# Kernel optimization log

Hardware: AMD Instinct MI355X
Metric: run time of the kernel (lower is better)

## Reference

```python
import jax, jax.numpy as jnp
import numpy as np

NUM_C = 100
DIM_S = 128
SIZE_M = 64
EMB = 128
MAX_CODE_LEN = 128
NODE_COUNT = 10000
PATH_COUNT = 10000
B, L = 16, 128


def setup_inputs() -> dict:
    key = jax.random.key(0)
    ks = jax.random.split(key, 24)
    def nrm(k, shape, fan):
        return jax.random.normal(k, shape, jnp.float32) * np.float32(np.sqrt(2.0 / fan))
    code = jax.random.randint(ks[0], (B, L, NUM_C * 2 + MAX_CODE_LEN * 3), 0, 10000)
    q = jax.random.randint(ks[1], (B, L), 0, NUM_C)
    r = jax.random.randint(ks[2], (B, L), 0, 2 * NUM_C)
    return {
        "code": code, "q": q, "r": r,
        "embed_nodes": nrm(ks[3], (NODE_COUNT + 2, EMB), EMB),
        "embed_paths": nrm(ks[4], (PATH_COUNT + 2, EMB), EMB),
        "W_pt": nrm(ks[5], (3 * EMB, 3 * EMB), 3 * EMB), "b_pt": jnp.zeros((3 * EMB,), jnp.float32),
        "W_att": nrm(ks[6], (3 * EMB, 1), 3 * EMB), "b_att": jnp.zeros((1,), jnp.float32),
        "k_emb": nrm(ks[7], (NUM_C + 1, DIM_S), DIM_S),
        "Mk": nrm(ks[8], (SIZE_M, DIM_S), DIM_S),
        "Mv0": nrm(ks[9], (SIZE_M, DIM_S), DIM_S),
        "v_emb": nrm(ks[10], (NUM_C * 2 + 2, DIM_S), DIM_S),
        "W_e": nrm(ks[11], (4 * DIM_S, DIM_S), 4 * DIM_S), "b_e": jnp.zeros((DIM_S,), jnp.float32),
        "W_a": nrm(ks[12], (4 * DIM_S, DIM_S), 4 * DIM_S), "b_a": jnp.zeros((DIM_S,), jnp.float32),
        "W_f": nrm(ks[13], (2 * DIM_S, DIM_S), 2 * DIM_S), "b_f": jnp.zeros((DIM_S,), jnp.float32),
        "W_p": nrm(ks[14], (DIM_S, 10), DIM_S), "b_p": jnp.zeros((10,), jnp.float32),
    }


def reference(code, q, r, embed_nodes, embed_paths, W_pt, b_pt, W_att, b_att,
              k_emb, Mk, Mv0, v_emb, W_e, b_e, W_a, b_a, W_f, b_f, W_p, b_p):
    bsz = code.shape[0]
    k = k_emb[q]                                    # [B,L,D]
    vr = v_emb[r]                                   # [B,L,D]
    # code2vec path triples: [B,L,MAX_CODE_LEN,3] = (start, path, end)
    c2v = code[:, :, NUM_C * 2:].reshape(bsz, code.shape[1], MAX_CODE_LEN, 3)
    full = jnp.concatenate([embed_nodes[c2v[..., 0]],
                            embed_nodes[c2v[..., 2]],
                            embed_paths[c2v[..., 1]]], axis=3)   # [B,L,P,3E]
    tr = jnp.tanh(full @ W_pt + b_pt)
    cw = tr @ W_att + b_att                          # [B,L,P,1]
    attn = jax.nn.softmax(cw, axis=1)                # faithful: softmax over seq dim (dim=1)
    code_vec = jnp.sum(full * attn, axis=2)          # [B,L,3E]
    v = jnp.concatenate([vr, code_vec], axis=2)      # [B,L,4D]
    w = jax.nn.softmax(k @ Mk.T, axis=-1)            # [B,L,M]
    e = jax.nn.sigmoid(v @ W_e + b_e)                # [B,L,D]
    a = jnp.tanh(v @ W_a + b_a)                      # [B,L,D]
    Mvt0 = jnp.broadcast_to(Mv0, (bsz,) + Mv0.shape) # [B,M,D]

    def step(Mvt, inp):
        et, at, wt = inp                             # [B,D],[B,D],[B,M]
        read = jnp.einsum('bm,bmd->bd', wt, Mvt)     # read pre-update memory (Mv[:, :-1])
        Mvt = Mvt * (1.0 - wt[:, :, None] * et[:, None, :]) + wt[:, :, None] * at[:, None, :]
        return Mvt, read

    _, reads = jax.lax.scan(step, Mvt0,
                            (e.transpose(1, 0, 2), a.transpose(1, 0, 2), w.transpose(1, 0, 2)))
    read = reads.transpose(1, 0, 2)                  # [B,L,D]
    f = jnp.tanh(jnp.concatenate([read, k], axis=-1) @ W_f + b_f)
    # dropout is identity in eval mode
    return jax.nn.sigmoid(f @ W_p + b_p)             # [B,L,10]
```

## Files before the change

kernel.cpp:

```cpp
#include <hip/hip_runtime.h>


typedef unsigned char u8;
typedef unsigned short u16;
typedef unsigned int u32;
typedef __attribute__((ext_vector_type(8))) short short8;
typedef __attribute__((ext_vector_type(4))) float f32x4;
typedef __attribute__((ext_vector_type(2))) float f32x2;

#define DEV __device__ __forceinline__
#define LOG2E 1.4426950408889634f
#define KSCALE 2.8853900817779268f

DEV u16 f2b(float f) {
    union { float f; u32 i; } v; v.f = f;
    u32 x = v.i;
    u32 r = (x + 0x7FFFu + ((x >> 16) & 1u)) >> 16;
    return (u16)r;
}
DEV float nexp(float x) { return __builtin_amdgcn_exp2f(x * LOG2E); }
DEV float nrcp(float x) { return __builtin_amdgcn_rcpf(x); }
DEV float fast_tanh(float x) {
    return 1.f - 2.f * nrcp(1.f + __builtin_amdgcn_exp2f(x * (2.f * LOG2E)));
}
DEV float sigmoidf_(float x) { return nrcp(1.f + __builtin_amdgcn_exp2f(-x * LOG2E)); }
DEV f32x2 d8(u32 x, bool hi) {
    return hi ? __builtin_amdgcn_cvt_pk_f32_fp8((int)x, true)
              : __builtin_amdgcn_cvt_pk_f32_fp8((int)x, false);
}
DEV u8 e8(float x) {
    return (u8)(__builtin_amdgcn_cvt_pk_fp8_f32(x, x, 0, false) & 0xFF);
}

__global__ void k_conv(const float* __restrict__ EN, const float* __restrict__ EP,
                       const float* __restrict__ Wpt, const float* __restrict__ We,
                       const float* __restrict__ Wa, const float* __restrict__ Wf,
                       const float* __restrict__ Wp,
                       const float* __restrict__ Kemb, const float* __restrict__ Mk,
                       u16* __restrict__ ENb, u16* __restrict__ EPb,
                       u8* __restrict__ EN8, u8* __restrict__ EP8,
                       u16* __restrict__ Wt, u16* __restrict__ WeaT,
                       u16* __restrict__ WfT, u16* __restrict__ WpT,
                       float* __restrict__ wsmall) {
    if (blockIdx.x >= 2048) {
        int wv = threadIdx.x >> 6, lane = threadIdx.x & 63;
        int row = (blockIdx.x - 2048) * 4 + wv;
        if (row >= 101) return;
        float lg = 0.f;
        for (int k = 0; k < 128; k += 8) {
            float mk8[8];
#pragma unroll
            for (int u = 0; u < 8; u++) mk8[u] = Mk[lane * 128 + k + u];
#pragma unroll
            for (int u = 0; u < 8; u++) lg = fmaf(Kemb[row * 128 + k + u], mk8[u], lg);
        }
        float mx = lg;
#pragma unroll
        for (int off = 32; off; off >>= 1) mx = fmaxf(mx, __shfl_xor(mx, off, 64));
        float ex = nexp(lg - mx);
        float sum = ex;
#pragma unroll
        for (int off = 32; off; off >>= 1) sum += __shfl_xor(sum, off, 64);
        wsmall[row * 64 + lane] = ex * nrcp(sum);
        return;
    }
    const int NEH = 10002 * 64;
    const int T0 = 2 * NEH;
    const int T1 = T0 + 147456;
    const int T2 = T1 + 131072;
    const int T3 = T2 + 32768;
    const int T4 = T3 + 2048;
    for (int i = blockIdx.x * blockDim.x + threadIdx.x; i < T4; i += 2048 * blockDim.x) {
        if (i < NEH) {
            float a = EN[2 * i], b = EN[2 * i + 1];
            ((u32*)ENb)[i] = ((u32)f2b(b) << 16) | f2b(a);
            ((u16*)EN8)[i] = (u16)__builtin_amdgcn_cvt_pk_fp8_f32(a, b, 0, false);
        } else if (i < T0) {
            int j = i - NEH;
            float a = EP[2 * j], b = EP[2 * j + 1];
            ((u32*)EPb)[j] = ((u32)f2b(b) << 16) | f2b(a);
            ((u16*)EP8)[j] = (u16)__builtin_amdgcn_cvt_pk_fp8_f32(a, b, 0, false);
        } else if (i < T1) {
            int w = i - T0;  u32 n = (u32)w / 384u, k = (u32)w % 384u;
            Wt[w] = f2b(Wpt[k * 384 + n]);
        } else if (i < T2) {
            int w = i - T1;  int n = w >> 9, k = w & 511;
            WeaT[w] = f2b((n < 128) ? We[k * 128 + n] : Wa[k * 128 + (n - 128)]);
        } else if (i < T3) {
            int w = i - T2;  int n = w >> 8, k = w & 255;
            WfT[w] = f2b(Wf[k * 128 + n]);
        } else {
            int w = i - T3;  int n = w >> 7, k = w & 127;
            WpT[w] = (n < 10) ? f2b(Wp[k * 10 + n]) : (u16)0;
        }
    }
}

__global__ void k_preM(const u16* __restrict__ ENb, const u16* __restrict__ EPb,
                       const u16* __restrict__ Wt, const float* __restrict__ bpt,
                       u8* __restrict__ PS8, u8* __restrict__ PE8, u8* __restrict__ PP8) {
    int which = blockIdx.y;
    int r0 = blockIdx.x * 32;
    int wv = threadIdx.x >> 6, lane = threadIdx.x & 63;
    int m = lane & 15, quad = lane >> 4;
    const u16* A = (which == 2) ? EPb : ENb;
    int koff = which * 128;
    u8* dst = (which == 0) ? PS8 : (which == 1) ? PE8 : PP8;

    short8 a[2][4];
#pragma unroll
    for (int rt = 0; rt < 2; rt++) {
        const short8* ap = (const short8*)(A + (r0 + rt * 16 + m) * 128 + quad * 8);
#pragma unroll
        for (int kc = 0; kc < 4; kc++) a[rt][kc] = ap[kc * 4];
    }

    for (int nt = 0; nt < 6; nt++) {
        int n0 = wv * 96 + nt * 16;
        const short8* bp = (const short8*)(Wt + (n0 + m) * 384 + koff + quad * 8);
        short8 b0 = bp[0], b1 = bp[4], b2 = bp[8], b3 = bp[12];
        int col = n0 + m;
        float bias = (which == 2) ? bpt[col] : 0.f;
#pragma unroll
        for (int rt = 0; rt < 2; rt++) {
            f32x4 acc = {0.f, 0.f, 0.f, 0.f};
            acc = __builtin_amdgcn_mfma_f32_16x16x32_bf16(a[rt][0], b0, acc, 0, 0, 0);
            acc = __builtin_amdgcn_mfma_f32_16x16x32_bf16(a[rt][1], b1, acc, 0, 0, 0);
            acc = __builtin_amdgcn_mfma_f32_16x16x32_bf16(a[rt][2], b2, acc, 0, 0, 0);
            acc = __builtin_amdgcn_mfma_f32_16x16x32_bf16(a[rt][3], b3, acc, 0, 0, 0);
#pragma unroll
            for (int reg = 0; reg < 4; reg++) {
                int row = r0 + rt * 16 + quad * 4 + reg;
                if (row < 10002) dst[row * 384 + col] = e8((acc[reg] + bias) * KSCALE);
            }
        }
    }
}

__global__ void k_cwsm(const int* __restrict__ code,
                       const u8* __restrict__ PS8, const u8* __restrict__ PE8,
                       const u8* __restrict__ PP8, const float* __restrict__ Watt,
                       float* __restrict__ attn) {
    int bp = blockIdx.x;
    int b = bp >> 7, p = bp & 127;
    int tid = threadIdx.x;
    int g = tid >> 4, gl = tid & 15;
    __shared__ float lgs[128];
    __shared__ float redm[4], reds[4];

    float w24[24];
    const float4* wp = (const float4*)(Watt + gl * 24);
#pragma unroll
    for (int u = 0; u < 6; u++) {
        float4 f = wp[u];
        w24[4 * u + 0] = -2.f * f.x; w24[4 * u + 1] = -2.f * f.y;
        w24[4 * u + 2] = -2.f * f.z; w24[4 * u + 3] = -2.f * f.w;
    }

    int si[8], pi[8], ei[8];
#pragma unroll
    for (int it = 0; it < 8; it++) {
        const int* c = code + ((b * 128 + g + it * 16) * 584 + 200 + 3 * p);
        si[it] = c[0]; pi[it] = c[1]; ei[it] = c[2];
    }

    uint2 cs0, cs1, cs2, ce0, ce1, ce2, cq0, cq1, cq2;
    {
        const uint2* bs = (const uint2*)(PS8 + si[0] * 384 + gl * 24);
        const uint2* be = (const uint2*)(PE8 + ei[0] * 384 + gl * 24);
        const uint2* bq = (const uint2*)(PP8 + pi[0] * 384 + gl * 24);
        cs0 = bs[0]; cs1 = bs[1]; cs2 = bs[2];
        ce0 = be[0]; ce1 = be[1]; ce2 = be[2];
        cq0 = bq[0]; cq1 = bq[1]; cq2 = bq[2];
    }
#pragma unroll
    for (int it = 0; it < 8; it++) {
        uint2 ns0, ns1, ns2, ne0, ne1, ne2, nq0, nq1, nq2;
        if (it < 7) {
            const uint2* bs = (const uint2*)(PS8 + si[it + 1] * 384 + gl * 24);
            const uint2* be = (const uint2*)(PE8 + ei[it + 1] * 384 + gl * 24);
            const uint2* bq = (const uint2*)(PP8 + pi[it + 1] * 384 + gl * 24);
            ns0 = bs[0]; ns1 = bs[1]; ns2 = bs[2];
            ne0 = be[0]; ne1 = be[1]; ne2 = be[2];
            nq0 = bq[0]; nq1 = bq[1]; nq2 = bq[2];
        }
        u32 sv[6] = { cs0.x, cs0.y, cs1.x, cs1.y, cs2.x, cs2.y };
        u32 ev[6] = { ce0.x, ce0.y, ce1.x, ce1.y, ce2.x, ce2.y };
        u32 qv[6] = { cq0.x, cq0.y, cq1.x, cq1.y, cq2.x, cq2.y };
        float acc = 0.f;
#pragma unroll
        for (int u = 0; u < 6; u++) {
            f32x2 zl = d8(sv[u], false) + d8(ev[u], false) + d8(qv[u], false);
            f32x2 zh = d8(sv[u], true)  + d8(ev[u], true)  + d8(qv[u], true);
            acc = fmaf(nrcp(1.f + __builtin_amdgcn_exp2f(zl.x)), w24[4 * u + 0], acc);
            acc = fmaf(nrcp(1.f + __builtin_amdgcn_exp2f(zl.y)), w24[4 * u + 1], acc);
            acc = fmaf(nrcp(1.f + __builtin_amdgcn_exp2f(zh.x)), w24[4 * u + 2], acc);
            acc = fmaf(nrcp(1.f + __builtin_amdgcn_exp2f(zh.y)), w24[4 * u + 3], acc);
        }
        acc += __shfl_xor(acc, 1, 64);
        acc += __shfl_xor(acc, 2, 64);
        acc += __shfl_xor(acc, 4, 64);
        acc += __shfl_xor(acc, 8, 64);
        if (gl == 0) lgs[g + it * 16] = acc;
        if (it < 7) {
            cs0 = ns0; cs1 = ns1; cs2 = ns2;
            ce0 = ne0; ce1 = ne1; ce2 = ne2;
            cq0 = nq0; cq1 = nq1; cq2 = nq2;
        }
    }
    __syncthreads();

    int lane = tid & 63, wvi = tid >> 6;
    float x = (tid < 128) ? lgs[tid] : -1e30f;
    float mx = x;
#pragma unroll
    for (int off = 32; off; off >>= 1) mx = fmaxf(mx, __shfl_xor(mx, off, 64));
    if (lane == 0) redm[wvi] = mx;
    __syncthreads();
    mx = fmaxf(redm[0], redm[1]);
    float ex = nexp(x - mx);
    float sum = ex;
#pragma unroll
    for (int off = 32; off; off >>= 1) sum += __shfl_xor(sum, off, 64);
    if (lane == 0) reds[wvi] = sum;
    __syncthreads();
    float inv = nrcp(reds[0] + reds[1]);
    if (tid < 128) attn[(b * 128 + tid) * 128 + p] = ex * inv;
}

__global__ void k_cv(const int* __restrict__ code, const float* __restrict__ attn,
                     const u8* __restrict__ EN8, const u8* __restrict__ EP8,
                     const int* __restrict__ rr, const int* __restrict__ qq,
                     const float* __restrict__ Vemb, const float* __restrict__ Kemb,
                     u16* __restrict__ vA, u16* __restrict__ fA) {
    int row = blockIdx.x;
    int tid = threadIdx.x;
    int wv = tid >> 6, lane = tid & 63;
    __shared__ int si[128], ei[128], pi[128];
    __shared__ float at[128];
    __shared__ float part[4][3][128];
    if (tid < 128) {
        const int* c = code + (row * 584 + 200);
        si[tid] = c[3 * tid]; pi[tid] = c[3 * tid + 1]; ei[tid] = c[3 * tid + 2];
        at[tid] = attn[row * 128 + tid];
    }
    if (tid < 128) {
        vA[row * 512 + tid] = f2b(Vemb[rr[row] * 128 + tid]);
    } else {
        int t2 = tid - 128;
        fA[row * 256 + 128 + t2] = f2b(Kemb[qq[row] * 128 + t2]);
    }
    __syncthreads();
    float a0 = 0.f, a1 = 0.f, b0 = 0.f, b1 = 0.f, c0 = 0.f, c1 = 0.f;
    int o = 2 * lane;

    u32 cur[6];
    {
        int p = wv, p2 = wv + 4;
        cur[0] = *(const u16*)(EN8 + si[p] * 128 + o);
        cur[1] = *(const u16*)(EN8 + ei[p] * 128 + o);
        cur[2] = *(const u16*)(EP8 + pi[p] * 128 + o);
        cur[3] = *(const u16*)(EN8 + si[p2] * 128 + o);
        cur[4] = *(const u16*)(EN8 + ei[p2] * 128 + o);
        cur[5] = *(const u16*)(EP8 + pi[p2] * 128 + o);
    }
#pragma unroll
    for (int it = 0; it < 16; it++) {
        int p = wv + it * 8;
        u32 nxt[6];
        if (it < 15) {
            int pn = p + 8, pn2 = p + 12;
            nxt[0] = *(const u16*)(EN8 + si[pn] * 128 + o);
            nxt[1] = *(const u16*)(EN8 + ei[pn] * 128 + o);
            nxt[2] = *(const u16*)(EP8 + pi[pn] * 128 + o);
            nxt[3] = *(const u16*)(EN8 + si[pn2] * 128 + o);
            nxt[4] = *(const u16*)(EN8 + ei[pn2] * 128 + o);
            nxt[5] = *(const u16*)(EP8 + pi[pn2] * 128 + o);
        }
        float w = at[p], w2 = at[p + 4];
        f32x2 fs = d8(cur[0], false), fe = d8(cur[1], false), fp = d8(cur[2], false);
        f32x2 gs = d8(cur[3], false), ge = d8(cur[4], false), gp = d8(cur[5], false);
        a0 = fmaf(w, fs.x, a0); a1 = fmaf(w, fs.y, a1);
        b0 = fmaf(w, fe.x, b0); b1 = fmaf(w, fe.y, b1);
        c0 = fmaf(w, fp.x, c0); c1 = fmaf(w, fp.y, c1);
        a0 = fmaf(w2, gs.x, a0); a1 = fmaf(w2, gs.y, a1);
        b0 = fmaf(w2, ge.x, b0); b1 = fmaf(w2, ge.y, b1);
        c0 = fmaf(w2, gp.x, c0); c1 = fmaf(w2, gp.y, c1);
        if (it < 15) {
#pragma unroll
            for (int z = 0; z < 6; z++) cur[z] = nxt[z];
        }
    }
    part[wv][0][2 * lane] = a0; part[wv][0][2 * lane + 1] = a1;
    part[wv][1][2 * lane] = b0; part[wv][1][2 * lane + 1] = b1;
    part[wv][2][2 * lane] = c0; part[wv][2][2 * lane + 1] = c1;
    __syncthreads();
    u16* vrow = vA + row * 512 + 128;
    for (int idx = tid; idx < 384; idx += 256) {
        int tbl = idx >> 7, col = idx & 127;
        vrow[idx] = f2b(part[0][tbl][col] + part[1][tbl][col] + part[2][tbl][col] + part[3][tbl][col]);
    }
}

__global__ void k_eawM(const u16* __restrict__ vA, const u16* __restrict__ WeaT,
                       const float* __restrict__ be, const float* __restrict__ ba,
                       float* __restrict__ eb, float* __restrict__ ab) {
    int rt = blockIdx.x >> 2, cg = blockIdx.x & 3;
    int wv = threadIdx.x >> 6, lane = threadIdx.x & 63;
    int ct = cg * 4 + wv;
    int m = lane & 15, quad = lane >> 4;
    const short8* ap = (const short8*)(vA + (rt * 16 + m) * 512 + quad * 8);
    const short8* bp = (const short8*)(WeaT + (ct * 16 + m) * 512 + quad * 8);
    f32x4 acc = {0.f, 0.f, 0.f, 0.f};
#pragma unroll
    for (int kc = 0; kc < 16; kc++)
        acc = __builtin_amdgcn_mfma_f32_16x16x32_bf16(ap[kc * 4], bp[kc * 4], acc, 0, 0, 0);
    int col = ct * 16 + m;
    bool isA = col >= 128;
    int c2 = isA ? col - 128 : col;
    float bias = isA ? ba[c2] : be[c2];
#pragma unroll
    for (int reg = 0; reg < 4; reg++) {
        int row = rt * 16 + quad * 4 + reg;
        float val = acc[reg] + bias;
        if (isA) ab[row * 128 + c2] = fast_tanh(val);
        else     eb[row * 128 + c2] = sigmoidf_(val);
    }
}

__global__ void k_scan(const float* __restrict__ Mv0, const float* __restrict__ eb,
                       const float* __restrict__ ab, const float* __restrict__ wsmall,
                       const int* __restrict__ qq, u16* __restrict__ fA) {
    int b = blockIdx.x >> 4, dblk = blockIdx.x & 15;
    int lane = threadIdx.x;
    int s = lane >> 3, dlo = lane & 7;
    int d = dblk * 8 + dlo;

    __shared__ float wsm[101 * 64];
    __shared__ float el[128][8];
    __shared__ float al[128][8];
    __shared__ int ql[128];

    for (int i = lane; i < 101 * 64; i += 64) wsm[i] = wsmall[i];
    for (int i = lane; i < 1024; i += 64) {
        int t = i >> 3, dl = i & 7;
        el[t][dl] = eb[(b * 128 + t) * 128 + dblk * 8 + dl];
        al[t][dl] = ab[(b * 128 + t) * 128 + dblk * 8 + dl];
    }
    for (int i = lane; i < 128; i += 64) ql[i] = qq[b * 128 + i];
    __syncthreads();

    float mv[8];
#pragma unroll
    for (int q = 0; q < 8; q++) mv[q] = Mv0[(s * 8 + q) * 128 + d];

    u16* fout = fA + (b * 128) * 256 + d;

    int qt = ql[0];
    const float4* wr = (const float4*)(wsm + qt * 64 + s * 8);
    float4 w0 = wr[0], w1 = wr[1];
    float ecur = el[0][dlo], acur = al[0][dlo];

    for (int t = 0; t < 128; t++) {
        int tn = (t < 127) ? t + 1 : 127;
        int qn = ql[tn];
        const float4* wrn = (const float4*)(wsm + qn * 64 + s * 8);
        float4 nw0 = wrn[0], nw1 = wrn[1];
        float en = el[tn][dlo], an = al[tn][dlo];

        float w[8] = { w0.x, w0.y, w0.z, w0.w, w1.x, w1.y, w1.z, w1.w };
        float rd = 0.f;
#pragma unroll
        for (int q = 0; q < 8; q++) {
            rd = fmaf(w[q], mv[q], rd);
            mv[q] = fmaf(w[q], fmaf(-mv[q], ecur, acur), mv[q]);
        }
        rd += __shfl_xor(rd, 8, 64);
        rd += __shfl_xor(rd, 16, 64);
        rd += __shfl_xor(rd, 32, 64);
        if (s == 0) fout[t * 256] = f2b(rd);

        ecur = en; acur = an; w0 = nw0; w1 = nw1;
    }
}

__global__ void k_outfin(const u16* __restrict__ fA, const u16* __restrict__ WfT,
                         const float* __restrict__ bfp, const u16* __restrict__ WpT,
                         const float* __restrict__ bp, float* __restrict__ out) {
    int rt = blockIdx.x;
    int wv = threadIdx.x >> 6, lane = threadIdx.x & 63;
    int m = lane & 15, quad = lane >> 4;
    __shared__ u16 ftile[16][128];

    const short8* ap = (const short8*)(fA + (rt * 16 + m) * 256 + quad * 8);
    const short8* bpw = (const short8*)(WfT + (wv * 16 + m) * 256 + quad * 8);
    f32x4 acc = {0.f, 0.f, 0.f, 0.f};
#pragma unroll
    for (int kc = 0; kc < 8; kc++)
        acc = __builtin_amdgcn_mfma_f32_16x16x32_bf16(ap[kc * 4], bpw[kc * 4], acc, 0, 0, 0);
    int col = wv * 16 + m;
    float bias = bfp[col];
#pragma unroll
    for (int reg = 0; reg < 4; reg++)
        ftile[quad * 4 + reg][col] = f2b(fast_tanh(acc[reg] + bias));
    __syncthreads();

    if (wv == 0) {
        f32x4 facc = {0.f, 0.f, 0.f, 0.f};
#pragma unroll
        for (int kc = 0; kc < 4; kc++) {
            short8 af = *(const short8*)(&ftile[m][kc * 32 + quad * 8]);
            short8 bf = *(const short8*)(WpT + m * 128 + kc * 32 + quad * 8);
            facc = __builtin_amdgcn_mfma_f32_16x16x32_bf16(af, bf, facc, 0, 0, 0);
        }
        if (m < 10) {
            float bias2 = bp[m];
#pragma unroll
            for (int reg = 0; reg < 4; reg++) {
                int row = rt * 16 + quad * 4 + reg;
                out[row * 10 + m] = sigmoidf_(facc[reg] + bias2);
            }
        }
    }
}

extern "C" void kernel_launch(void* const* d_in, const int* in_sizes, int n_in,
                              void* d_out, int out_size, void* d_ws, size_t ws_size,
                              hipStream_t stream) {
    const int*   code = (const int*)d_in[0];
    const int*   q    = (const int*)d_in[1];
    const int*   r    = (const int*)d_in[2];
    const float* EN   = (const float*)d_in[3];
    const float* EP   = (const float*)d_in[4];
    const float* Wpt  = (const float*)d_in[5];
    const float* bpt  = (const float*)d_in[6];
    const float* Watt = (const float*)d_in[7];
    const float* Kemb = (const float*)d_in[9];
    const float* Mk   = (const float*)d_in[10];
    const float* Mv0  = (const float*)d_in[11];
    const float* Vemb = (const float*)d_in[12];
    const float* We   = (const float*)d_in[13];
    const float* be   = (const float*)d_in[14];
    const float* Wa   = (const float*)d_in[15];
    const float* ba   = (const float*)d_in[16];
    const float* Wf   = (const float*)d_in[17];
    const float* bf_  = (const float*)d_in[18];
    const float* Wp   = (const float*)d_in[19];
    const float* bp   = (const float*)d_in[20];

    char* ws = (char*)d_ws;
    size_t off = 0;
    auto alloc = [&](size_t bytes) { void* p = ws + off; off = (off + bytes + 255) & ~255UL; return p; };
    u8*    PS8    = (u8*)alloc(10002UL * 384);
    u8*    PE8    = (u8*)alloc(10002UL * 384);
    u8*    PP8    = (u8*)alloc(10002UL * 384);
    u16*   ENb    = (u16*)alloc(10016UL * 128 * 2);
    u16*   EPb    = (u16*)alloc(10016UL * 128 * 2);
    u8*    EN8    = (u8*)alloc(10002UL * 128);
    u8*    EP8    = (u8*)alloc(10002UL * 128);
    u16*   Wt     = (u16*)alloc(384UL * 384 * 2);
    u16*   WeaT   = (u16*)alloc(256UL * 512 * 2);
    u16*   WfT    = (u16*)alloc(128UL * 256 * 2);
    u16*   WpT    = (u16*)alloc(16UL * 128 * 2);
    float* attn   = (float*)alloc(16UL * 128 * 128 * 4);
    u16*   vA     = (u16*)alloc(2048UL * 512 * 2);
    u16*   fA     = (u16*)alloc(2048UL * 256 * 2);
    float* eb     = (float*)alloc(2048UL * 128 * 4);
    float* ab     = (float*)alloc(2048UL * 128 * 4);
    float* wsmall = (float*)alloc(101UL * 64 * 4);

    k_conv<<<2048 + 26, 256, 0, stream>>>(EN, EP, Wpt, We, Wa, Wf, Wp, Kemb, Mk,
                                          ENb, EPb, EN8, EP8, Wt, WeaT, WfT, WpT, wsmall);
    k_preM<<<dim3(313, 3), 256, 0, stream>>>(ENb, EPb, Wt, bpt, PS8, PE8, PP8);
    k_cwsm<<<2048, 256, 0, stream>>>(code, PS8, PE8, PP8, Watt, attn);
    k_cv<<<2048, 256, 0, stream>>>(code, attn, EN8, EP8, r, q, Vemb, Kemb, vA, fA);
    k_eawM<<<512, 256, 0, stream>>>(vA, WeaT, be, ba, eb, ab);
    k_scan<<<256, 64, 0, stream>>>(Mv0, eb, ab, wsmall, q, fA);
    k_outfin<<<128, 512, 0, stream>>>(fA, WfT, bf_, WpT, bp, (float*)d_out);
}
```

Before: 224.0 us.

## Widen gather loads, coalesce weight transpose reads, merge sigmoid reciprocals

Weight conversion now reads the source matrices with coalesced accesses and scatters the transposed bf16 writes, instead of strided reads. The attention-logit kernel loads each 24-byte fp8 slice as one 16-byte plus one 8-byte load instead of three 8-byte loads. It also pairs two sigmoid terms so they share a single reciprocal. The code-vector kernel has each lane gather 4 fp8 bytes (32-lane halves per path) instead of 2, doubling the partial-sum slots in shared memory. These target load instruction count and transcendental throughput, at the cost of uncoalesced writes in prep and a slightly larger reduction.

```diff
diff --git a/kernel.cpp b/kernel.cpp
--- a/kernel.cpp
+++ b/kernel.cpp
@@ -67,8 +67,9 @@
     const int NEH = 10002 * 64;
     const int T0 = 2 * NEH;
     const int T1 = T0 + 147456;
-    const int T2 = T1 + 131072;
-    const int T3 = T2 + 32768;
+    const int T2 = T1 + 65536;
+    const int T2b = T2 + 65536;
+    const int T3 = T2b + 32768;
     const int T4 = T3 + 2048;
     for (int i = blockIdx.x * blockDim.x + threadIdx.x; i < T4; i += 2048 * blockDim.x) {
         if (i < NEH) {
@@ -81,14 +82,18 @@
             ((u32*)EPb)[j] = ((u32)f2b(b) << 16) | f2b(a);
             ((u16*)EP8)[j] = (u16)__builtin_amdgcn_cvt_pk_fp8_f32(a, b, 0, false);
         } else if (i < T1) {
-            int w = i - T0;  u32 n = (u32)w / 384u, k = (u32)w % 384u;
-            Wt[w] = f2b(Wpt[k * 384 + n]);
+            int w = i - T0;
+            u32 k = (u32)w / 384u, n = (u32)w % 384u;
+            Wt[n * 384 + k] = f2b(Wpt[w]);
         } else if (i < T2) {
-            int w = i - T1;  int n = w >> 9, k = w & 511;
-            WeaT[w] = f2b((n < 128) ? We[k * 128 + n] : Wa[k * 128 + (n - 128)]);
+            int w = i - T1;  int k = w >> 7, n = w & 127;
+            WeaT[n * 512 + k] = f2b(We[w]);
+        } else if (i < T2b) {
+            int w = i - T2;  int k = w >> 7, n = w & 127;
+            WeaT[(128 + n) * 512 + k] = f2b(Wa[w]);
         } else if (i < T3) {
-            int w = i - T2;  int n = w >> 8, k = w & 255;
-            WfT[w] = f2b(Wf[k * 128 + n]);
+            int w = i - T2b; int k = w >> 7, n = w & 127;
+            WfT[n * 256 + k] = f2b(Wf[w]);
         } else {
             int w = i - T3;  int n = w >> 7, k = w & 127;
             WpT[w] = (n < 10) ? f2b(Wp[k * 10 + n]) : (u16)0;
@@ -164,38 +169,42 @@
         si[it] = c[0]; pi[it] = c[1]; ei[it] = c[2];
     }
 
-    uint2 cs0, cs1, cs2, ce0, ce1, ce2, cq0, cq1, cq2;
+    uint4 cs4, ce4, cq4; uint2 cs2, ce2, cq2;
     {
-        const uint2* bs = (const uint2*)(PS8 + si[0] * 384 + gl * 24);
-        const uint2* be = (const uint2*)(PE8 + ei[0] * 384 + gl * 24);
-        const uint2* bq = (const uint2*)(PP8 + pi[0] * 384 + gl * 24);
-        cs0 = bs[0]; cs1 = bs[1]; cs2 = bs[2];
-        ce0 = be[0]; ce1 = be[1]; ce2 = be[2];
-        cq0 = bq[0]; cq1 = bq[1]; cq2 = bq[2];
+        const u8* bs = PS8 + si[0] * 384 + gl * 24;
+        const u8* be = PE8 + ei[0] * 384 + gl * 24;
+        const u8* bq = PP8 + pi[0] * 384 + gl * 24;
+        cs4 = *(const uint4*)bs; cs2 = *(const uint2*)(bs + 16);
+        ce4 = *(const uint4*)be; ce2 = *(const uint2*)(be + 16);
+        cq4 = *(const uint4*)bq; cq2 = *(const uint2*)(bq + 16);
     }
 #pragma unroll
     for (int it = 0; it < 8; it++) {
-        uint2 ns0, ns1, ns2, ne0, ne1, ne2, nq0, nq1, nq2;
+        uint4 ns4, ne4, nq4; uint2 ns2, ne2, nq2;
         if (it < 7) {
-            const uint2* bs = (const uint2*)(PS8 + si[it + 1] * 384 + gl * 24);
-            const uint2* be = (const uint2*)(PE8 + ei[it + 1] * 384 + gl * 24);
-            const uint2* bq = (const uint2*)(PP8 + pi[it + 1] * 384 + gl * 24);
-            ns0 = bs[0]; ns1 = bs[1]; ns2 = bs[2];
-            ne0 = be[0]; ne1 = be[1]; ne2 = be[2];
-            nq0 = bq[0]; nq1 = bq[1]; nq2 = bq[2];
-        }
-        u32 sv[6] = { cs0.x, cs0.y, cs1.x, cs1.y, cs2.x, cs2.y };
-        u32 ev[6] = { ce0.x, ce0.y, ce1.x, ce1.y, ce2.x, ce2.y };
-        u32 qv[6] = { cq0.x, cq0.y, cq1.x, cq1.y, cq2.x, cq2.y };
+            const u8* bs = PS8 + si[it + 1] * 384 + gl * 24;
+            const u8* be = PE8 + ei[it + 1] * 384 + gl * 24;
+            const u8* bq = PP8 + pi[it + 1] * 384 + gl * 24;
+            ns4 = *(const uint4*)bs; ns2 = *(const uint2*)(bs + 16);
+            ne4 = *(const uint4*)be; ne2 = *(const uint2*)(be + 16);
+            nq4 = *(const uint4*)bq; nq2 = *(const uint2*)(bq + 16);
+        }
+        u32 sv[6] = { cs4.x, cs4.y, cs4.z, cs4.w, cs2.x, cs2.y };
+        u32 ev[6] = { ce4.x, ce4.y, ce4.z, ce4.w, ce2.x, ce2.y };
+        u32 qv[6] = { cq4.x, cq4.y, cq4.z, cq4.w, cq2.x, cq2.y };
         float acc = 0.f;
 #pragma unroll
         for (int u = 0; u < 6; u++) {
             f32x2 zl = d8(sv[u], false) + d8(ev[u], false) + d8(qv[u], false);
             f32x2 zh = d8(sv[u], true)  + d8(ev[u], true)  + d8(qv[u], true);
-            acc = fmaf(nrcp(1.f + __builtin_amdgcn_exp2f(zl.x)), w24[4 * u + 0], acc);
-            acc = fmaf(nrcp(1.f + __builtin_amdgcn_exp2f(zl.y)), w24[4 * u + 1], acc);
-            acc = fmaf(nrcp(1.f + __builtin_amdgcn_exp2f(zh.x)), w24[4 * u + 2], acc);
-            acc = fmaf(nrcp(1.f + __builtin_amdgcn_exp2f(zh.y)), w24[4 * u + 3], acc);
+            float d0 = 1.f + __builtin_amdgcn_exp2f(zl.x);
+            float d1 = 1.f + __builtin_amdgcn_exp2f(zl.y);
+            float d2 = 1.f + __builtin_amdgcn_exp2f(zh.x);
+            float d3 = 1.f + __builtin_amdgcn_exp2f(zh.y);
+            float n01 = fmaf(w24[4 * u + 0], d1, w24[4 * u + 1] * d0);
+            float n23 = fmaf(w24[4 * u + 2], d3, w24[4 * u + 3] * d2);
+            acc = fmaf(n01, nrcp(d0 * d1), acc);
+            acc = fmaf(n23, nrcp(d2 * d3), acc);
         }
         acc += __shfl_xor(acc, 1, 64);
         acc += __shfl_xor(acc, 2, 64);
@@ -203,9 +212,9 @@
         acc += __shfl_xor(acc, 8, 64);
         if (gl == 0) lgs[g + it * 16] = acc;
         if (it < 7) {
-            cs0 = ns0; cs1 = ns1; cs2 = ns2;
-            ce0 = ne0; ce1 = ne1; ce2 = ne2;
-            cq0 = nq0; cq1 = nq1; cq2 = nq2;
+            cs4 = ns4; cs2 = ns2;
+            ce4 = ne4; ce2 = ne2;
+            cq4 = nq4; cq2 = nq2;
         }
     }
     __syncthreads();
@@ -236,9 +245,10 @@
     int row = blockIdx.x;
     int tid = threadIdx.x;
     int wv = tid >> 6, lane = tid & 63;
+    int h = lane >> 5, cl = lane & 31;
     __shared__ int si[128], ei[128], pi[128];
     __shared__ float at[128];
-    __shared__ float part[4][3][128];
+    __shared__ float part[8][3][128];
     if (tid < 128) {
         const int* c = code + (row * 584 + 200);
         si[tid] = c[3 * tid]; pi[tid] = c[3 * tid + 1]; ei[tid] = c[3 * tid + 2];
@@ -251,54 +261,48 @@
         fA[row * 256 + 128 + t2] = f2b(Kemb[qq[row] * 128 + t2]);
     }
     __syncthreads();
-    float a0 = 0.f, a1 = 0.f, b0 = 0.f, b1 = 0.f, c0 = 0.f, c1 = 0.f;
-    int o = 2 * lane;
-
-    u32 cur[6];
-    {
-        int p = wv, p2 = wv + 4;
-        cur[0] = *(const u16*)(EN8 + si[p] * 128 + o);
-        cur[1] = *(const u16*)(EN8 + ei[p] * 128 + o);
-        cur[2] = *(const u16*)(EP8 + pi[p] * 128 + o);
-        cur[3] = *(const u16*)(EN8 + si[p2] * 128 + o);
-        cur[4] = *(const u16*)(EN8 + ei[p2] * 128 + o);
-        cur[5] = *(const u16*)(EP8 + pi[p2] * 128 + o);
-    }
+
+    int o = cl * 4;
+    int pb = wv + h * 4;
+    float a0 = 0.f, a1 = 0.f, a2 = 0.f, a3 = 0.f;
+    float b0 = 0.f, b1 = 0.f, b2 = 0.f, b3 = 0.f;
+    float c0 = 0.f, c1 = 0.f, c2 = 0.f, c3 = 0.f;
+
+    u32 cur0, cur1, cur2;
+    cur0 = *(const u32*)(EN8 + si[pb] * 128 + o);
+    cur1 = *(const u32*)(EN8 + ei[pb] * 128 + o);
+    cur2 = *(const u32*)(EP8 + pi[pb] * 128 + o);
 #pragma unroll
     for (int it = 0; it < 16; it++) {
-        int p = wv + it * 8;
-        u32 nxt[6];
+        int p = pb + it * 8;
+        u32 n0, n1, n2;
         if (it < 15) {
-            int pn = p + 8, pn2 = p + 12;
-            nxt[0] = *(const u16*)(EN8 + si[pn] * 128 + o);
-            nxt[1] = *(const u16*)(EN8 + ei[pn] * 128 + o);
-            nxt[2] = *(const u16*)(EP8 + pi[pn] * 128 + o);
-            nxt[3] = *(const u16*)(EN8 + si[pn2] * 128 + o);
-            nxt[4] = *(const u16*)(EN8 + ei[pn2] * 128 + o);
-            nxt[5] = *(const u16*)(EP8 + pi[pn2] * 128 + o);
-        }
-        float w = at[p], w2 = at[p + 4];
-        f32x2 fs = d8(cur[0], false), fe = d8(cur[1], false), fp = d8(cur[2], false);
-        f32x2 gs = d8(cur[3], false), ge = d8(cur[4], false), gp = d8(cur[5], false);
-        a0 = fmaf(w, fs.x, a0); a1 = fmaf(w, fs.y, a1);
-        b0 = fmaf(w, fe.x, b0); b1 = fmaf(w, fe.y, b1);
-        c0 = fmaf(w, fp.x, c0); c1 = fmaf(w, fp.y, c1);
-        a0 = fmaf(w2, gs.x, a0); a1 = fmaf(w2, gs.y, a1);
-        b0 = fmaf(w2, ge.x, b0); b1 = fmaf(w2, ge.y, b1);
-        c0 = fmaf(w2, gp.x, c0); c1 = fmaf(w2, gp.y, c1);
-        if (it < 15) {
-#pragma unroll
-            for (int z = 0; z < 6; z++) cur[z] = nxt[z];
-        }
-    }
-    part[wv][0][2 * lane] = a0; part[wv][0][2 * lane + 1] = a1;
-    part[wv][1][2 * lane] = b0; part[wv][1][2 * lane + 1] = b1;
-    part[wv][2][2 * lane] = c0; part[wv][2][2 * lane + 1] = c1;
+            int pn = p + 8;
+            n0 = *(const u32*)(EN8 + si[pn] * 128 + o);
+            n1 = *(const u32*)(EN8 + ei[pn] * 128 + o);
+            n2 = *(const u32*)(EP8 + pi[pn] * 128 + o);
+        }
+        float w = at[p];
+        f32x2 sl = d8(cur0, false), sh = d8(cur0, true);
+        f32x2 el = d8(cur1, false), eh = d8(cur1, true);
+        f32x2 pl = d8(cur2, false), ph = d8(cur2, true);
+        a0 = fmaf(w, sl.x, a0); a1 = fmaf(w, sl.y, a1); a2 = fmaf(w, sh.x, a2); a3 = fmaf(w, sh.y, a3);
+        b0 = fmaf(w, el.x, b0); b1 = fmaf(w, el.y, b1); b2 = fmaf(w, eh.x, b2); b3 = fmaf(w, eh.y, b3);
+        c0 = fmaf(w, pl.x, c0); c1 = fmaf(w, pl.y, c1); c2 = fmaf(w, ph.x, c2); c3 = fmaf(w, ph.y, c3);
+        if (it < 15) { cur0 = n0; cur1 = n1; cur2 = n2; }
+    }
+    int slot = wv * 2 + h;
+    part[slot][0][o + 0] = a0; part[slot][0][o + 1] = a1; part[slot][0][o + 2] = a2; part[slot][0][o + 3] = a3;
+    part[slot][1][o + 0] = b0; part[slot][1][o + 1] = b1; part[slot][1][o + 2] = b2; part[slot][1][o + 3] = b3;
+    part[slot][2][o + 0] = c0; part[slot][2][o + 1] = c1; part[slot][2][o + 2] = c2; part[slot][2][o + 3] = c3;
     __syncthreads();
     u16* vrow = vA + row * 512 + 128;
     for (int idx = tid; idx < 384; idx += 256) {
         int tbl = idx >> 7, col = idx & 127;
-        vrow[idx] = f2b(part[0][tbl][col] + part[1][tbl][col] + part[2][tbl][col] + part[3][tbl][col]);
+        float s = 0.f;
+#pragma unroll
+        for (int sl2 = 0; sl2 < 8; sl2++) s += part[sl2][tbl][col];
+        vrow[idx] = f2b(s);
     }
 }
 
```

After: 222.4 us. No clear change (-0.7%).
